# Optimization experiments

Measured on AMD Instinct MI355X. Metric: run time of the kernel, lower is better.

Reference implementation:

```python
import jax, jax.numpy as jnp
import numpy as np

N, S, D_MODEL, H = 8, 1024, 1024, 16
D = D_MODEL // H
NEG = -1e9


def setup_inputs() -> dict:
    key = jax.random.key(0)
    ks = jax.random.split(key, 12)
    s = 0.02
    q = jax.random.normal(ks[0], (N, S, D_MODEL), jnp.float32)
    k = jax.random.normal(ks[1], (N, S, D_MODEL), jnp.float32)
    v = jax.random.normal(ks[2], (N, S, D_MODEL), jnp.float32)
    # causal mask: 1 where masked (strict upper triangle)
    causal_mask = jnp.triu(jnp.ones((S, S), jnp.int32), k=1)
    # padding mask: 1 where key position is padding
    padding_mask = jax.random.randint(ks[3], (N, S), 0, 2, jnp.int32)
    Wq = jax.random.normal(ks[4], (D_MODEL, D_MODEL), jnp.float32) * s
    bq = jnp.zeros((D_MODEL,), jnp.float32)
    Wk = jax.random.normal(ks[5], (D_MODEL, D_MODEL), jnp.float32) * s
    bk = jnp.zeros((D_MODEL,), jnp.float32)
    Wv = jax.random.normal(ks[6], (D_MODEL, D_MODEL), jnp.float32) * s
    bv = jnp.zeros((D_MODEL,), jnp.float32)
    Wo = jax.random.normal(ks[7], (D_MODEL, D_MODEL), jnp.float32) * s
    bo = jnp.zeros((D_MODEL,), jnp.float32)
    return {"q": q, "k": k, "v": v, "causal_mask": causal_mask,
            "padding_mask": padding_mask, "Wq": Wq, "bq": bq, "Wk": Wk,
            "bk": bk, "Wv": Wv, "bv": bv, "Wo": Wo, "bo": bo}


def reference(q, k, v, causal_mask, padding_mask, Wq, bq, Wk, bk, Wv, bv, Wo, bo):
    n, qs, _ = q.shape
    # projections (nn.Linear: x @ W.T + b)
    qp = (q @ Wq.T + bq).reshape(n, qs, H, D).transpose(0, 2, 1, 3)  # [N,H,qS,D]
    kp = (k @ Wk.T + bk).reshape(n, -1, H, D).transpose(0, 2, 1, 3)  # [N,H,kS,D]
    vp = (v @ Wv.T + bv).reshape(n, -1, H, D).transpose(0, 2, 1, 3)  # [N,H,kS,D]
    # NOTE: faithful to source -- scale by sqrt(d_model), not sqrt(d_head)
    score = jnp.einsum('bhqd,bhkd->bhqk', qp, kp) / jnp.sqrt(jnp.float32(D_MODEL))
    score = jnp.where(causal_mask[None, None, :, :] == 1, NEG, score)
    score = jnp.where(padding_mask[:, None, None, :] == 1, NEG, score)
    w = jax.nn.softmax(score, axis=-1)  # dropout is identity in eval mode
    x = jnp.einsum('bhqk,bhkd->bhqd', w, vp)  # [N,H,qS,D]
    x = x.transpose(0, 2, 1, 3).reshape(n, qs, D_MODEL)
    x = x @ Wo.T + bo
    return (x, w)
```

## Files before the change

### kernel.cpp

```cpp
#include <hip/hip_runtime.h>

typedef __bf16 bf16;
typedef bf16 bf16x8 __attribute__((ext_vector_type(8)));
typedef bf16 bf16x4 __attribute__((ext_vector_type(4)));
typedef float f32x4 __attribute__((ext_vector_type(4)));

#define S_LEN 1024
#define DM    1024
#define NH    16
#define HD    64
#define NB    8
#define NEGV  (-1e9f)
#define QSCALE 0.03125f

#define EPI_HEADS 0
#define EPI_VT    1
#define EPI_OUT   2

__device__ __forceinline__ void async16(const bf16* g, const bf16* l) {
    __builtin_amdgcn_global_load_lds(
        (const __attribute__((address_space(1))) void*)g,
        (__attribute__((address_space(3))) void*)l, 16, 0, 0);
}

__global__ __launch_bounds__(256) void cast_all(
    const float* __restrict__ q, const float* __restrict__ k,
    const float* __restrict__ v, const float* __restrict__ wq,
    const float* __restrict__ wk, const float* __restrict__ wv,
    const float* __restrict__ wo, bf16* __restrict__ out)
{
    size_t idx = ((size_t)blockIdx.x * 256 + threadIdx.x) * 4;
    const float* src;
    size_t soff;
    if (idx < 25165824) {
        int seg = (int)(idx >> 23);
        soff = idx & 8388607;
        src = seg == 0 ? q : (seg == 1 ? k : v);
    } else {
        size_t r = idx - 25165824;
        int seg = (int)(r >> 20);
        soff = r & 1048575;
        src = seg == 0 ? wq : (seg == 1 ? wk : (seg == 2 ? wv : wo));
    }
    f32x4 val = *(const f32x4*)&src[soff];
    bf16x4 o = {(bf16)val.x, (bf16)val.y, (bf16)val.z, (bf16)val.w};
    *(bf16x4*)&out[idx] = o;
}

__global__ __launch_bounds__(256) void gemm_qkv(
    const bf16* __restrict__ Ap, const bf16* __restrict__ Ball,
    const float* __restrict__ bq, const float* __restrict__ bk,
    const float* __restrict__ bv, bf16* __restrict__ Qp,
    bf16* __restrict__ Kp, bf16* __restrict__ VpT)
{
    __shared__ bf16 As[128][32];
    __shared__ bf16 Bs[128][32];

    const int tid    = threadIdx.x;
    const int l      = tid & 63;
    const int wid    = tid >> 6;
    const int wr     = wid >> 1, wc = wid & 1;
    const int lane15 = l & 15, quad = l >> 4;
    const int row0   = blockIdx.x * 128;
    const int seg    = blockIdx.y >> 3;
    const int col0   = (blockIdx.y & 7) * 128;
    const int brow0  = seg * 1024 + col0;

    const bf16* Aseg = Ap + (size_t)seg * 8388608;
    const float* bias = seg == 0 ? bq : (seg == 1 ? bk : bv);

    f32x4 acc[4][4];
    #pragma unroll
    for (int i = 0; i < 4; ++i)
        #pragma unroll
        for (int j = 0; j < 4; ++j)
            acc[i][j] = (f32x4){0.f, 0.f, 0.f, 0.f};

    for (int k0 = 0; k0 < 1024; k0 += 32) {
        #pragma unroll
        for (int j = 0; j < 2; ++j) {
            int cbase = j * 256 + wid * 64;
            int c = cbase + l;
            int r = c >> 2, kc = (c & 3) << 3;
            async16(&Aseg[(size_t)(row0 + r) * 1024 + k0 + kc], &As[0][0] + cbase * 8);
            async16(&Ball[(size_t)(brow0 + r) * 1024 + k0 + kc], &Bs[0][0] + cbase * 8);
        }
        __syncthreads();

        bf16x8 afr[4], bfr[4];
        #pragma unroll
        for (int tm = 0; tm < 4; ++tm)
            afr[tm] = *(const bf16x8*)&As[wr * 64 + tm * 16 + lane15][quad * 8];
        #pragma unroll
        for (int tn = 0; tn < 4; ++tn)
            bfr[tn] = *(const bf16x8*)&Bs[wc * 64 + tn * 16 + lane15][quad * 8];
        #pragma unroll
        for (int tm = 0; tm < 4; ++tm)
            #pragma unroll
            for (int tn = 0; tn < 4; ++tn)
                acc[tm][tn] = __builtin_amdgcn_mfma_f32_16x16x32_bf16(
                    afr[tm], bfr[tn], acc[tm][tn], 0, 0, 0);
        __syncthreads();
    }

    #pragma unroll
    for (int tm = 0; tm < 4; ++tm) {
        #pragma unroll
        for (int tn = 0; tn < 4; ++tn) {
            #pragma unroll
            for (int i = 0; i < 4; ++i) {
                int gr = row0 + wr * 64 + tm * 16 + quad * 4 + i;
                int gc = col0 + wc * 64 + tn * 16 + lane15;
                float vout = acc[tm][tn][i] + bias[gc];
                int n = gr >> 10, s = gr & 1023, h = gc >> 6, d = gc & 63;
                if (seg == 0) {
                    Qp[(((size_t)(n * NH + h) * S_LEN + s) << 6) + d] = (bf16)(vout * QSCALE);
                } else if (seg == 1) {
                    Kp[(((size_t)(n * NH + h) * S_LEN + s) << 6) + d] = (bf16)vout;
                } else {
                    VpT[(((size_t)(n * NH + h) * HD + d) << 10) + s] = (bf16)vout;
                }
            }
        }
    }
}

template<int EPI>
__global__ __launch_bounds__(256) void gemm_nt(
    const bf16* __restrict__ Ap, const bf16* __restrict__ Bp,
    const float* __restrict__ bias, void* __restrict__ Cp)
{
    __shared__ bf16 As[128][32];
    __shared__ bf16 Bs[128][32];

    const int tid    = threadIdx.x;
    const int l      = tid & 63;
    const int wid    = tid >> 6;
    const int wr     = wid >> 1, wc = wid & 1;
    const int lane15 = l & 15, quad = l >> 4;
    const int row0   = blockIdx.x * 128;
    const int col0   = blockIdx.y * 128;

    f32x4 acc[4][4];
    #pragma unroll
    for (int i = 0; i < 4; ++i)
        #pragma unroll
        for (int j = 0; j < 4; ++j)
            acc[i][j] = (f32x4){0.f, 0.f, 0.f, 0.f};

    for (int k0 = 0; k0 < 1024; k0 += 32) {
        #pragma unroll
        for (int j = 0; j < 2; ++j) {
            int cbase = j * 256 + wid * 64;
            int c = cbase + l;
            int r = c >> 2, kc = (c & 3) << 3;
            async16(&Ap[(size_t)(row0 + r) * 1024 + k0 + kc], &As[0][0] + cbase * 8);
            async16(&Bp[(size_t)(col0 + r) * 1024 + k0 + kc], &Bs[0][0] + cbase * 8);
        }
        __syncthreads();

        bf16x8 afr[4], bfr[4];
        #pragma unroll
        for (int tm = 0; tm < 4; ++tm)
            afr[tm] = *(const bf16x8*)&As[wr * 64 + tm * 16 + lane15][quad * 8];
        #pragma unroll
        for (int tn = 0; tn < 4; ++tn)
            bfr[tn] = *(const bf16x8*)&Bs[wc * 64 + tn * 16 + lane15][quad * 8];
        #pragma unroll
        for (int tm = 0; tm < 4; ++tm)
            #pragma unroll
            for (int tn = 0; tn < 4; ++tn)
                acc[tm][tn] = __builtin_amdgcn_mfma_f32_16x16x32_bf16(
                    afr[tm], bfr[tn], acc[tm][tn], 0, 0, 0);
        __syncthreads();
    }

    #pragma unroll
    for (int tm = 0; tm < 4; ++tm) {
        #pragma unroll
        for (int tn = 0; tn < 4; ++tn) {
            #pragma unroll
            for (int i = 0; i < 4; ++i) {
                int gr = row0 + wr * 64 + tm * 16 + quad * 4 + i;
                int gc = col0 + wc * 64 + tn * 16 + lane15;
                float vout = acc[tm][tn][i] + bias[gc];
                if constexpr (EPI == EPI_HEADS) {
                    int n = gr >> 10, s = gr & 1023, h = gc >> 6, d = gc & 63;
                    ((bf16*)Cp)[(((size_t)(n * NH + h) * S_LEN + s) << 6) + d] = (bf16)vout;
                } else if constexpr (EPI == EPI_VT) {
                    int n = gr >> 10, s = gr & 1023, h = gc >> 6, d = gc & 63;
                    ((bf16*)Cp)[(((size_t)(n * NH + h) * HD + d) << 10) + s] = (bf16)vout;
                } else {
                    ((float*)Cp)[(size_t)gr * DM + gc] = vout;
                }
            }
        }
    }
}

__global__ __launch_bounds__(256, 4) void attn_fused(
    const bf16* __restrict__ Qp, const bf16* __restrict__ Kp,
    const bf16* __restrict__ VpT, const int* __restrict__ pad,
    float* __restrict__ Wout, bf16* __restrict__ ctx)
{
    const int gid   = blockIdx.x;
    const int xcd   = gid & 7;
    const int t_    = gid >> 3;
    const int qblk  = t_ & 63;
    const int bh    = ((t_ >> 6) << 3) | xcd;
    const int h = bh & 15, n = bh >> 4;

    const bf16* Qb = Qp + (size_t)bh * S_LEN * HD;
    const bf16* Kb = Kp + (size_t)bh * S_LEN * HD;
    const bf16* Vb = VpT + (size_t)bh * HD * S_LEN;
    float* Wb = Wout + (size_t)bh * S_LEN * S_LEN;

    const int tid = threadIdx.x;
    const int l = tid & 63, wid = tid >> 6;
    const int lane15 = l & 15, quad = l >> 4;
    const int q0 = qblk * 16;
    const int q = q0 + lane15;
    const int qmax = q0 + 15;

    __shared__ bf16  P[16][1032];
    __shared__ float redM[4][16];
    __shared__ float redS[4][16];

    bf16x8 qf0 = *(const bf16x8*)&Qb[(size_t)q * HD + quad * 8];
    bf16x8 qf1 = *(const bf16x8*)&Qb[(size_t)q * HD + 32 + quad * 8];

    const int keyw = wid * 256;
    f32x4 sc[16];
    float mm = NEGV;

    #pragma unroll
    for (int t = 0; t < 16; ++t) {
        int kb = keyw + t * 16;
        if (kb <= qmax) {
            bf16x8 kf0 = *(const bf16x8*)&Kb[(size_t)(kb + lane15) * HD + quad * 8];
            bf16x8 kf1 = *(const bf16x8*)&Kb[(size_t)(kb + lane15) * HD + 32 + quad * 8];
            f32x4 a = (f32x4){0.f, 0.f, 0.f, 0.f};
            a = __builtin_amdgcn_mfma_f32_16x16x32_bf16(kf0, qf0, a, 0, 0, 0);
            a = __builtin_amdgcn_mfma_f32_16x16x32_bf16(kf1, qf1, a, 0, 0, 0);
            int4 pd = *(const int4*)&pad[n * S_LEN + kb + quad * 4];
            const int* pdi = (const int*)&pd;
            int key0 = kb + quad * 4;
            #pragma unroll
            for (int i = 0; i < 4; ++i)
                a[i] = (key0 + i > q || pdi[i] != 0) ? NEGV : a[i];
            sc[t] = a;
            mm = fmaxf(mm, fmaxf(fmaxf(a[0], a[1]), fmaxf(a[2], a[3])));
        }
    }

    mm = fmaxf(mm, __shfl_xor(mm, 16));
    mm = fmaxf(mm, __shfl_xor(mm, 32));
    if (l < 16) redM[wid][l] = mm;
    __syncthreads();
    float m = fmaxf(fmaxf(redM[0][lane15], redM[1][lane15]),
                    fmaxf(redM[2][lane15], redM[3][lane15]));

    float vskip = __expf(NEGV - m);

    float sm = 0.f;
    #pragma unroll
    for (int t = 0; t < 16; ++t) {
        int kb = keyw + t * 16;
        if (kb <= qmax) {
            #pragma unroll
            for (int i = 0; i < 4; ++i) {
                float p = __expf(sc[t][i] - m);
                sc[t][i] = p;
                sm += p;
            }
        } else {
            sm += 4.f * vskip;
        }
    }
    sm += __shfl_xor(sm, 16);
    sm += __shfl_xor(sm, 32);
    if (l < 16) redS[wid][l] = sm;
    __syncthreads();
    float inv = 1.f / (redS[0][lane15] + redS[1][lane15] +
                       redS[2][lane15] + redS[3][lane15]);
    float wskip = vskip * inv;
    bool anyDeg = __ballot(m == NEGV) != 0;

    #pragma unroll
    for (int t = 0; t < 16; ++t) {
        int kb = keyw + t * 16;
        int off = kb + quad * 4;
        if (kb <= qmax) {
            f32x4 wv = {sc[t][0] * inv, sc[t][1] * inv,
                        sc[t][2] * inv, sc[t][3] * inv};
            *(f32x4*)&Wb[(size_t)q * S_LEN + off] = wv;
            bf16x4 pb = {(bf16)wv.x, (bf16)wv.y, (bf16)wv.z, (bf16)wv.w};
            *(bf16x4*)&P[lane15][off] = pb;
        } else {
            f32x4 wv = {wskip, wskip, wskip, wskip};
            *(f32x4*)&Wb[(size_t)q * S_LEN + off] = wv;
            bf16 pv = (bf16)wskip;
            bf16x4 pb = {pv, pv, pv, pv};
            *(bf16x4*)&P[lane15][off] = pb;
        }
    }
    __syncthreads();

    const int dbase = wid * 16;
    const int cEnd = anyDeg ? 32 : ((qmax >> 5) + 1);
    f32x4 o = (f32x4){0.f, 0.f, 0.f, 0.f};
    #pragma unroll 4
    for (int c = 0; c < cEnd; ++c) {
        bf16x8 a = *(const bf16x8*)&P[lane15][c * 32 + quad * 8];
        bf16x8 b = *(const bf16x8*)&Vb[(size_t)(dbase + lane15) * S_LEN + c * 32 + quad * 8];
        o = __builtin_amdgcn_mfma_f32_16x16x32_bf16(a, b, o, 0, 0, 0);
    }
    #pragma unroll
    for (int i = 0; i < 4; ++i) {
        int row = q0 + quad * 4 + i;
        ctx[((size_t)(n * S_LEN + row) << 10) + h * HD + dbase + lane15] = (bf16)o[i];
    }
}

extern "C" void kernel_launch(void* const* d_in, const int* in_sizes, int n_in,
                              void* d_out, int out_size, void* d_ws, size_t ws_size,
                              hipStream_t stream)
{
    const float* q   = (const float*)d_in[0];
    const float* k   = (const float*)d_in[1];
    const float* v   = (const float*)d_in[2];
    const int*   pad = (const int*)  d_in[4];
    const float* Wq  = (const float*)d_in[5];
    const float* bq  = (const float*)d_in[6];
    const float* Wk  = (const float*)d_in[7];
    const float* bk  = (const float*)d_in[8];
    const float* Wv  = (const float*)d_in[9];
    const float* bv  = (const float*)d_in[10];
    const float* Wo  = (const float*)d_in[11];
    const float* bo  = (const float*)d_in[12];

    float* x_out = (float*)d_out;
    float* w_out = x_out + (size_t)NB * S_LEN * DM;

    bf16* wsb = (bf16*)d_ws;
    bf16* Qc  = wsb;
    bf16* Wqb = wsb + 25165824;
    bf16* Wob = wsb + 28311552;
    bf16* Qp  = wsb + 29360128;
    bf16* Kp  = wsb + 37748736;
    bf16* VpT = wsb + 46137344;
    bf16* ctx = wsb + 54525952;

    cast_all<<<28672, 256, 0, stream>>>(q, k, v, Wq, Wk, Wv, Wo, wsb);

    gemm_qkv<<<dim3(64, 24), 256, 0, stream>>>(Qc, Wqb, bq, bk, bv, Qp, Kp, VpT);

    attn_fused<<<dim3(8192), 256, 0, stream>>>(Qp, Kp, VpT, pad, w_out, ctx);

    gemm_nt<EPI_OUT><<<dim3(64, 8), 256, 0, stream>>>(ctx, Wob, bo, x_out);
}
```

Measured before the change: 930.9 us.

## Store V in blocked 8-seq layout and interleave key tiles across waves

```diff
diff --git a/kernel.cpp b/kernel.cpp
--- a/kernel.cpp
+++ b/kernel.cpp
@@ -14,7 +14,6 @@
 #define QSCALE 0.03125f
 
 #define EPI_HEADS 0
-#define EPI_VT    1
 #define EPI_OUT   2
 
 __device__ __forceinline__ void async16(const bf16* g, const bf16* l) {
@@ -51,7 +50,7 @@
     const bf16* __restrict__ Ap, const bf16* __restrict__ Ball,
     const float* __restrict__ bq, const float* __restrict__ bk,
     const float* __restrict__ bv, bf16* __restrict__ Qp,
-    bf16* __restrict__ Kp, bf16* __restrict__ VpT)
+    bf16* __restrict__ Kp, bf16* __restrict__ Vp8)
 {
     __shared__ bf16 As[128][32];
     __shared__ bf16 Bs[128][32];
@@ -107,18 +106,26 @@
     for (int tm = 0; tm < 4; ++tm) {
         #pragma unroll
         for (int tn = 0; tn < 4; ++tn) {
-            #pragma unroll
-            for (int i = 0; i < 4; ++i) {
-                int gr = row0 + wr * 64 + tm * 16 + quad * 4 + i;
-                int gc = col0 + wc * 64 + tn * 16 + lane15;
-                float vout = acc[tm][tn][i] + bias[gc];
-                int n = gr >> 10, s = gr & 1023, h = gc >> 6, d = gc & 63;
-                if (seg == 0) {
-                    Qp[(((size_t)(n * NH + h) * S_LEN + s) << 6) + d] = (bf16)(vout * QSCALE);
-                } else if (seg == 1) {
-                    Kp[(((size_t)(n * NH + h) * S_LEN + s) << 6) + d] = (bf16)vout;
-                } else {
-                    VpT[(((size_t)(n * NH + h) * HD + d) << 10) + s] = (bf16)vout;
+            int gr0 = row0 + wr * 64 + tm * 16 + quad * 4;
+            int gc  = col0 + wc * 64 + tn * 16 + lane15;
+            if (seg == 2) {
+                int n = gr0 >> 10, s0 = gr0 & 1023, h = gc >> 6, d = gc & 63;
+                float b = bias[gc];
+                bf16x4 ov = {(bf16)(acc[tm][tn][0] + b), (bf16)(acc[tm][tn][1] + b),
+                             (bf16)(acc[tm][tn][2] + b), (bf16)(acc[tm][tn][3] + b)};
+                *(bf16x4*)&Vp8[(size_t)(n * NH + h) * 65536 +
+                               (size_t)(s0 >> 3) * 512 + d * 8 + (s0 & 7)] = ov;
+            } else {
+                #pragma unroll
+                for (int i = 0; i < 4; ++i) {
+                    int gr = gr0 + i;
+                    float vout = acc[tm][tn][i] + bias[gc];
+                    int n = gr >> 10, s = gr & 1023, h = gc >> 6, d = gc & 63;
+                    if (seg == 0) {
+                        Qp[(((size_t)(n * NH + h) * S_LEN + s) << 6) + d] = (bf16)(vout * QSCALE);
+                    } else {
+                        Kp[(((size_t)(n * NH + h) * S_LEN + s) << 6) + d] = (bf16)vout;
+                    }
                 }
             }
         }
@@ -187,9 +194,6 @@
                 if constexpr (EPI == EPI_HEADS) {
                     int n = gr >> 10, s = gr & 1023, h = gc >> 6, d = gc & 63;
                     ((bf16*)Cp)[(((size_t)(n * NH + h) * S_LEN + s) << 6) + d] = (bf16)vout;
-                } else if constexpr (EPI == EPI_VT) {
-                    int n = gr >> 10, s = gr & 1023, h = gc >> 6, d = gc & 63;
-                    ((bf16*)Cp)[(((size_t)(n * NH + h) * HD + d) << 10) + s] = (bf16)vout;
                 } else {
                     ((float*)Cp)[(size_t)gr * DM + gc] = vout;
                 }
@@ -200,7 +204,7 @@
 
 __global__ __launch_bounds__(256, 4) void attn_fused(
     const bf16* __restrict__ Qp, const bf16* __restrict__ Kp,
-    const bf16* __restrict__ VpT, const int* __restrict__ pad,
+    const bf16* __restrict__ Vp8, const int* __restrict__ pad,
     float* __restrict__ Wout, bf16* __restrict__ ctx)
 {
     const int gid   = blockIdx.x;
@@ -212,7 +216,7 @@
 
     const bf16* Qb = Qp + (size_t)bh * S_LEN * HD;
     const bf16* Kb = Kp + (size_t)bh * S_LEN * HD;
-    const bf16* Vb = VpT + (size_t)bh * HD * S_LEN;
+    const bf16* Vb = Vp8 + (size_t)bh * HD * S_LEN;
     float* Wb = Wout + (size_t)bh * S_LEN * S_LEN;
 
     const int tid = threadIdx.x;
@@ -229,13 +233,14 @@
     bf16x8 qf0 = *(const bf16x8*)&Qb[(size_t)q * HD + quad * 8];
     bf16x8 qf1 = *(const bf16x8*)&Qb[(size_t)q * HD + 32 + quad * 8];
 
-    const int keyw = wid * 256;
     f32x4 sc[16];
     float mm = NEGV;
 
+    #define KB_OF(t) ((((((t) >> 1) << 3) + (wid << 1) + ((t) & 1))) << 4)
+
     #pragma unroll
     for (int t = 0; t < 16; ++t) {
-        int kb = keyw + t * 16;
+        int kb = KB_OF(t);
         if (kb <= qmax) {
             bf16x8 kf0 = *(const bf16x8*)&Kb[(size_t)(kb + lane15) * HD + quad * 8];
             bf16x8 kf1 = *(const bf16x8*)&Kb[(size_t)(kb + lane15) * HD + 32 + quad * 8];
@@ -265,7 +270,7 @@
     float sm = 0.f;
     #pragma unroll
     for (int t = 0; t < 16; ++t) {
-        int kb = keyw + t * 16;
+        int kb = KB_OF(t);
         if (kb <= qmax) {
             #pragma unroll
             for (int i = 0; i < 4; ++i) {
@@ -288,7 +293,7 @@
 
     #pragma unroll
     for (int t = 0; t < 16; ++t) {
-        int kb = keyw + t * 16;
+        int kb = KB_OF(t);
         int off = kb + quad * 4;
         if (kb <= qmax) {
             f32x4 wv = {sc[t][0] * inv, sc[t][1] * inv,
@@ -304,6 +309,7 @@
             *(bf16x4*)&P[lane15][off] = pb;
         }
     }
+    #undef KB_OF
     __syncthreads();
 
     const int dbase = wid * 16;
@@ -312,7 +318,7 @@
     #pragma unroll 4
     for (int c = 0; c < cEnd; ++c) {
         bf16x8 a = *(const bf16x8*)&P[lane15][c * 32 + quad * 8];
-        bf16x8 b = *(const bf16x8*)&Vb[(size_t)(dbase + lane15) * S_LEN + c * 32 + quad * 8];
+        bf16x8 b = *(const bf16x8*)&Vb[((size_t)(c * 4 + quad) * 64 + dbase + lane15) * 8];
         o = __builtin_amdgcn_mfma_f32_16x16x32_bf16(a, b, o, 0, 0, 0);
     }
     #pragma unroll
@@ -348,14 +354,14 @@
     bf16* Wob = wsb + 28311552;
     bf16* Qp  = wsb + 29360128;
     bf16* Kp  = wsb + 37748736;
-    bf16* VpT = wsb + 46137344;
+    bf16* Vp8 = wsb + 46137344;
     bf16* ctx = wsb + 54525952;
 
     cast_all<<<28672, 256, 0, stream>>>(q, k, v, Wq, Wk, Wv, Wo, wsb);
 
-    gemm_qkv<<<dim3(64, 24), 256, 0, stream>>>(Qc, Wqb, bq, bk, bv, Qp, Kp, VpT);
-
-    attn_fused<<<dim3(8192), 256, 0, stream>>>(Qp, Kp, VpT, pad, w_out, ctx);
+    gemm_qkv<<<dim3(64, 24), 256, 0, stream>>>(Qc, Wqb, bq, bk, bv, Qp, Kp, Vp8);
+
+    attn_fused<<<dim3(8192), 256, 0, stream>>>(Qp, Kp, Vp8, pad, w_out, ctx);
 
     gemm_nt<EPI_OUT><<<dim3(64, 8), 256, 0, stream>>>(ctx, Wob, bo, x_out);
 }
```

Result: faster. 877.5 us (-5.7%).
